# Kernel tuning notes

Hardware: AMD Instinct MI355X
Metric: run time of the kernel (lower is better)

The kernel has to match this reference:

```python
import jax, jax.numpy as jnp
import numpy as np

N_NODES = 100000
N_EDGES = 6400000


def setup_inputs() -> dict:
    key = jax.random.key(0)
    k1, k2, k3, k4, k5, k6 = jax.random.split(key, 6)
    x = jax.random.normal(k1, (N_NODES, 10), dtype=jnp.float32)
    edge_index = jax.random.randint(k2, (2, N_EDGES), 0, N_NODES, dtype=jnp.int64)
    # GCNConv(10,16) and GCNConv(16,2) parameters (glorot-ish scale)
    W1 = jax.random.normal(k3, (10, 16), dtype=jnp.float32) * (1.0 / np.sqrt(10))
    b1 = jnp.zeros((16,), dtype=jnp.float32)
    W2 = jax.random.normal(k4, (16, 2), dtype=jnp.float32) * (1.0 / np.sqrt(16))
    b2 = jnp.zeros((2,), dtype=jnp.float32)
    return {"x": x, "edge_index": edge_index, "W1": W1, "b1": b1, "W2": W2, "b2": b2}


def _gcn_conv(h, src, dst, norm, W, b, n_nodes):
    # PyG GCNConv: linear first, then normalized scatter-add aggregation
    h = h @ W                                   # [N, out]
    msg = h[src] * norm[:, None]                # gather + per-edge scale
    out = jax.ops.segment_sum(msg, dst, num_segments=n_nodes)
    return out + b


def reference(x, edge_index, W1, b1, W2, b2):
    n_nodes = x.shape[0]
    loop = jnp.arange(n_nodes, dtype=edge_index.dtype)
    src = jnp.concatenate([edge_index[0], loop])  # self-loops added (PyG default)
    dst = jnp.concatenate([edge_index[1], loop])
    # symmetric normalization deg^{-1/2} A_hat deg^{-1/2} (deg from target index)
    deg = jax.ops.segment_sum(jnp.ones_like(dst, dtype=x.dtype), dst, num_segments=n_nodes)
    dinv = jnp.where(deg > 0, jax.lax.rsqrt(deg), 0.0)
    norm = dinv[src] * dinv[dst]                 # [E+N]
    h = _gcn_conv(x, src, dst, norm, W1, b1, n_nodes)
    h = jax.nn.relu(h)
    out = _gcn_conv(h, src, dst, norm, W2, b2, n_nodes)
    return out
```

## Files before the change

kernel.cpp:

```cpp
#include <hip/hip_runtime.h>
#include <hip/hip_fp16.h>


#define BKT_BITS  8
#define BKT_SZ    256
#define NBK       512
#define TPB_A     1024
#define TPB_B     1024
#define CHUNK     25600
#define NIT       (CHUNK / TPB_A)
#define DST_SHIFT 24
#define SRC_MASK  0xFFFFFFu
#define XS_BYTES  32
#define SENTINEL  0xFFFFFFFFu

static __device__ __forceinline__ int nt_src(const void* ei, int is64, int n_edges, unsigned e) {
    return is64 ? (int)__builtin_nontemporal_load(&((const long long*)ei)[e])
                : __builtin_nontemporal_load(&((const int*)ei)[e]);
}
static __device__ __forceinline__ int nt_dst(const void* ei, int is64, int n_edges, unsigned e) {
    return is64 ? (int)__builtin_nontemporal_load(&((const long long*)ei)[(unsigned)n_edges + e])
                : __builtin_nontemporal_load(&((const int*)ei)[(unsigned)n_edges + e]);
}

static __device__ __forceinline__ float2 h2f(unsigned w) {
    __half2 h = *(__half2*)&w;
    return __half22float2(h);
}

static __global__ void detect_init_kernel(const unsigned int* __restrict__ w, int* flag,
                                          unsigned* __restrict__ gbase, unsigned cap) {
    __shared__ int nz;
    if (threadIdx.x == 0) nz = 0;
    __syncthreads();
    int local = 0;
    for (int k = threadIdx.x; k < 4096; k += blockDim.x)
        if (w[2 * k + 1] != 0u) local = 1;
    if (local) atomicOr(&nz, 1);
    __syncthreads();
    if (threadIdx.x == 0) *flag = (nz == 0) ? 1 : 0;
    for (int b = threadIdx.x; b < NBK; b += blockDim.x)
        gbase[b] = (unsigned)b * cap;
}

static __global__ void scatterB_kernel(const void* __restrict__ ei, const int* __restrict__ flag,
                                       unsigned* __restrict__ gbase,
                                       unsigned* __restrict__ bucketed,
                                       int n_edges, unsigned cap) {
    __shared__ unsigned short dlo[CHUNK];
    __shared__ unsigned dbit[CHUNK / 32];
    __shared__ unsigned h[NBK];
    __shared__ unsigned runbase[NBK];
    __shared__ unsigned cur[NBK];
    const int t = threadIdx.x;
    const unsigned e0 = (unsigned)blockIdx.x * CHUNK;
    const int is64 = *flag;
    for (int i = t; i < NBK; i += TPB_A) h[i] = 0u;
    __syncthreads();
    for (int it = 0; it < NIT; ++it) {
        unsigned idx = (unsigned)it * TPB_A + (unsigned)t;
        unsigned e = e0 + idx;
        bool valid = e < (unsigned)n_edges;
        unsigned d = valid ? (unsigned)nt_dst(ei, is64, n_edges, e) : 0u;
        dlo[idx] = (unsigned short)d;
        unsigned long long m = __ballot((d >> 16) & 1u);
        if ((t & 31) == 0)
            dbit[idx >> 5] = (unsigned)(((t & 63) >= 32) ? (m >> 32) : m);
        if (valid) atomicAdd(&h[d >> BKT_BITS], 1u);
    }
    __syncthreads();
    for (int b = t; b < NBK; b += TPB_A) {
        unsigned hb = h[b];
        unsigned rb = 0u;
        if (hb) rb = atomicAdd(&gbase[b], (hb + 15u) & ~15u);
        runbase[b] = rb;
        cur[b] = rb;
    }
    __syncthreads();
    for (int it = 0; it < NIT; ++it) {
        unsigned idx = (unsigned)it * TPB_A + (unsigned)t;
        unsigned e = e0 + idx;
        if (e < (unsigned)n_edges) {
            unsigned s = (unsigned)nt_src(ei, is64, n_edges, e);
            unsigned d = (unsigned)dlo[idx] | (((dbit[idx >> 5] >> (idx & 31u)) & 1u) << 16);
            unsigned b = d >> BKT_BITS;
            unsigned pos = atomicAdd(&cur[b], 1u);
            if (pos < (b + 1u) * cap)
                bucketed[pos] = s | ((d & (BKT_SZ - 1u)) << DST_SHIFT);
        }
    }
    __syncthreads();
    for (int b = t; b < NBK; b += TPB_A) {
        if (!h[b]) continue;
        unsigned rb = runbase[b];
        unsigned lim = (b + 1u) * cap;
        unsigned cu = cur[b]; if (cu > lim) cu = lim;
        unsigned end = rb + ((cu - rb + 15u) & ~15u);
        if (end > lim) end = lim;
        for (unsigned q = cu; q < end; ++q) bucketed[q] = SENTINEL;
    }
}

static __global__ void passB_kernel(const unsigned* __restrict__ bucketed,
                                    const unsigned* __restrict__ gbase, unsigned cap,
                                    const float* __restrict__ x,
                                    unsigned* __restrict__ csr_src,
                                    unsigned* __restrict__ row_start,
                                    unsigned* __restrict__ cnt,
                                    float* __restrict__ dinv,
                                    char* __restrict__ xs, int n_nodes) {
    const int b = blockIdx.x;
    const int n0 = b << BKT_BITS;
    const int t = threadIdx.x;
    const unsigned base = (unsigned)b * cap;
    unsigned gb = gbase[b];
    unsigned lim = base + cap;
    if (gb > lim) gb = lim;
    const unsigned count = gb - base;

    __shared__ unsigned h4[4][BKT_SZ];
    __shared__ unsigned s0[BKT_SZ], s1[BKT_SZ];
    __shared__ unsigned cur[BKT_SZ];
    for (int i = t; i < 4 * BKT_SZ; i += TPB_B) ((unsigned*)h4)[i] = 0u;
    __syncthreads();
    const int copy = (t >> 8) & 3;
    const uint4* B4 = (const uint4*)(bucketed + base);
    const unsigned nquad = count >> 2;
    for (unsigned q = t; q < nquad; q += TPB_B) {
        uint4 w4 = B4[q];
        if (w4.x != SENTINEL) atomicAdd(&h4[copy][w4.x >> DST_SHIFT], 1u);
        if (w4.y != SENTINEL) atomicAdd(&h4[copy][w4.y >> DST_SHIFT], 1u);
        if (w4.z != SENTINEL) atomicAdd(&h4[copy][w4.z >> DST_SHIFT], 1u);
        if (w4.w != SENTINEL) atomicAdd(&h4[copy][w4.w >> DST_SHIFT], 1u);
    }
    __syncthreads();
    unsigned hv = 0;
    unsigned* a = s0; unsigned* c = s1;
    if (t < BKT_SZ) {
        hv = h4[0][t] + h4[1][t] + h4[2][t] + h4[3][t];
        a[t] = hv;
    }
    __syncthreads();
    for (int off = 1; off < BKT_SZ; off <<= 1) {
        if (t < BKT_SZ) c[t] = a[t] + (t >= off ? a[t - off] : 0u);
        __syncthreads();
        unsigned* tmp = a; a = c; c = tmp;
    }
    if (t < BKT_SZ) {
        unsigned excl = a[t] - hv;
        cur[t] = excl;
        int n = n0 + t;
        if (n < n_nodes) {
            row_start[n] = base + excl;
            cnt[n] = hv;
            float di = rsqrtf((float)(hv + 1u));
            dinv[n] = di;
            unsigned w[5];
#pragma unroll
            for (int j = 0; j < 5; j++) {
                unsigned lo = __half_as_ushort(__float2half_rn(x[(size_t)n * 10 + 2 * j] * di));
                unsigned hi = __half_as_ushort(__float2half_rn(x[(size_t)n * 10 + 2 * j + 1] * di));
                w[j] = lo | (hi << 16);
            }
            char* row = xs + (size_t)n * XS_BYTES;
            *(uint4*)row = make_uint4(w[0], w[1], w[2], w[3]);
            *(uint2*)(row + 16) = make_uint2(w[4], 0u);
        }
    }
    __syncthreads();
    for (unsigned q = t; q < nquad; q += TPB_B) {
        uint4 w4 = B4[q];
        if (w4.x != SENTINEL) {
            unsigned pos = base + atomicAdd(&cur[w4.x >> DST_SHIFT], 1u);
            csr_src[pos] = w4.x & SRC_MASK;
        }
        if (w4.y != SENTINEL) {
            unsigned pos = base + atomicAdd(&cur[w4.y >> DST_SHIFT], 1u);
            csr_src[pos] = w4.y & SRC_MASK;
        }
        if (w4.z != SENTINEL) {
            unsigned pos = base + atomicAdd(&cur[w4.z >> DST_SHIFT], 1u);
            csr_src[pos] = w4.z & SRC_MASK;
        }
        if (w4.w != SENTINEL) {
            unsigned pos = base + atomicAdd(&cur[w4.w >> DST_SHIFT], 1u);
            csr_src[pos] = w4.w & SRC_MASK;
        }
    }
}

static __global__ void node1_kernel(const float* __restrict__ x, const float* __restrict__ dinv,
                                    char* __restrict__ xs, int n_nodes) {
    int i = blockIdx.x * blockDim.x + threadIdx.x;
    if (i >= n_nodes) return;
    float di = dinv[i];
    unsigned w[5];
#pragma unroll
    for (int j = 0; j < 5; j++) {
        unsigned lo = __half_as_ushort(__float2half_rn(x[(size_t)i * 10 + 2 * j] * di));
        unsigned hi = __half_as_ushort(__float2half_rn(x[(size_t)i * 10 + 2 * j + 1] * di));
        w[j] = lo | (hi << 16);
    }
    char* row = xs + (size_t)i * XS_BYTES;
    *(uint4*)row = make_uint4(w[0], w[1], w[2], w[3]);
    *(uint2*)(row + 16) = make_uint2(w[4], 0u);
}

static __global__ void gather1_kernel(const unsigned int* __restrict__ row_start,
                                      const unsigned int* __restrict__ cnt,
                                      const unsigned int* __restrict__ csr_src,
                                      const char* __restrict__ xs,
                                      const float* __restrict__ dinv,
                                      const float* __restrict__ W1, const float* __restrict__ b1,
                                      const float* __restrict__ W2,
                                      float* __restrict__ gs, int n_nodes) {
    __shared__ float sW1[160];
    __shared__ float sb1[16];
    __shared__ float sW2[32];
    for (int k = threadIdx.x; k < 160; k += blockDim.x) sW1[k] = W1[k];
    if (threadIdx.x < 16) sb1[threadIdx.x] = b1[threadIdx.x];
    if (threadIdx.x < 32) sW2[threadIdx.x] = W2[threadIdx.x];
    __syncthreads();
    int node = blockIdx.x * (blockDim.x >> 4) + (threadIdx.x >> 4);
    int lg = threadIdx.x & 15;
    if (node >= n_nodes) return;
    unsigned start = row_start[node];
    unsigned degn = cnt[node];
    float acc[10];
#pragma unroll
    for (int j = 0; j < 10; j++) acc[j] = 0.f;
    for (unsigned k = lg; k < degn; k += 16) {
        unsigned s = csr_src[start + k];
        const char* row = xs + (size_t)s * XS_BYTES;
        uint4 a = *(const uint4*)row;
        unsigned b = *(const unsigned*)(row + 16);
        float2 f;
        f = h2f(a.x); acc[0] += f.x; acc[1] += f.y;
        f = h2f(a.y); acc[2] += f.x; acc[3] += f.y;
        f = h2f(a.z); acc[4] += f.x; acc[5] += f.y;
        f = h2f(a.w); acc[6] += f.x; acc[7] += f.y;
        f = h2f(b);   acc[8] += f.x; acc[9] += f.y;
    }
    if (lg == 0) {
        const char* row = xs + (size_t)node * XS_BYTES;
        uint4 a = *(const uint4*)row;
        unsigned b = *(const unsigned*)(row + 16);
        float2 f;
        f = h2f(a.x); acc[0] += f.x; acc[1] += f.y;
        f = h2f(a.y); acc[2] += f.x; acc[3] += f.y;
        f = h2f(a.z); acc[4] += f.x; acc[5] += f.y;
        f = h2f(a.w); acc[6] += f.x; acc[7] += f.y;
        f = h2f(b);   acc[8] += f.x; acc[9] += f.y;
    }
#pragma unroll
    for (int off = 8; off > 0; off >>= 1) {
#pragma unroll
        for (int j = 0; j < 10; j++) acc[j] += __shfl_xor(acc[j], off);
    }
    float di = dinv[node];
    float h = sb1[lg];
#pragma unroll
    for (int k = 0; k < 10; k++) h = fmaf(acc[k] * di, sW1[k * 16 + lg], h);
    h = fmaxf(h, 0.f);
    float g0 = h * sW2[lg * 2 + 0];
    float g1 = h * sW2[lg * 2 + 1];
#pragma unroll
    for (int off = 8; off > 0; off >>= 1) {
        g0 += __shfl_xor(g0, off);
        g1 += __shfl_xor(g1, off);
    }
    if (lg == 0) {
        float2 o;
        o.x = g0 * di;
        o.y = g1 * di;
        ((float2*)gs)[node] = o;
    }
}

static __global__ void gather2_kernel(const unsigned int* __restrict__ row_start,
                                      const unsigned int* __restrict__ cnt,
                                      const unsigned int* __restrict__ csr_src,
                                      const float* __restrict__ gs,
                                      const float* __restrict__ dinv,
                                      const float* __restrict__ b2,
                                      float* __restrict__ out, int n_nodes) {
    int node = blockIdx.x * (blockDim.x >> 4) + (threadIdx.x >> 4);
    int lg = threadIdx.x & 15;
    if (node >= n_nodes) return;
    unsigned start = row_start[node];
    unsigned degn = cnt[node];
    float a0 = 0.f, a1 = 0.f;
    const float2* G = (const float2*)gs;
    for (unsigned k = lg; k < degn; k += 16) {
        float2 v = G[csr_src[start + k]];
        a0 += v.x; a1 += v.y;
    }
    if (lg == 0) {
        float2 s = G[node];
        a0 += s.x; a1 += s.y;
    }
#pragma unroll
    for (int off = 8; off > 0; off >>= 1) {
        a0 += __shfl_xor(a0, off);
        a1 += __shfl_xor(a1, off);
    }
    if (lg == 0) {
        float di = dinv[node];
        float2 o;
        o.x = fmaf(a0, di, b2[0]);
        o.y = fmaf(a1, di, b2[1]);
        ((float2*)out)[node] = o;
    }
}

static __global__ void deg_kernel(const void* __restrict__ ei, const int* __restrict__ flag,
                                  unsigned int* __restrict__ cnt, int n_edges) {
    const int is64 = *flag;
    unsigned stride = gridDim.x * blockDim.x;
    for (unsigned e = blockIdx.x * blockDim.x + threadIdx.x; e < (unsigned)n_edges; e += stride) {
        int d = nt_dst(ei, is64, n_edges, e);
        atomicAdd(&cnt[d], 1u);
    }
}
static __global__ void alloc_kernel(const unsigned int* __restrict__ cnt,
                                    unsigned int* __restrict__ row_start,
                                    unsigned int* __restrict__ cursor,
                                    unsigned int* __restrict__ gcur,
                                    float* __restrict__ dinv, int n_nodes) {
    __shared__ unsigned wsum[4];
    int i = blockIdx.x * blockDim.x + threadIdx.x;
    int lane = threadIdx.x & 63;
    int wid = threadIdx.x >> 6;
    unsigned d = (i < n_nodes) ? cnt[i] : 0u;
    unsigned scan = d;
#pragma unroll
    for (int off = 1; off < 64; off <<= 1) {
        unsigned t = __shfl_up(scan, off);
        if (lane >= off) scan += t;
    }
    if (lane == 63) wsum[wid] = scan;
    __syncthreads();
    if (threadIdx.x == 0) {
        unsigned s0 = wsum[0], s1 = wsum[1], s2 = wsum[2], s3 = wsum[3];
        unsigned base = atomicAdd(gcur, s0 + s1 + s2 + s3);
        wsum[0] = base;
        wsum[1] = base + s0;
        wsum[2] = base + s0 + s1;
        wsum[3] = base + s0 + s1 + s2;
    }
    __syncthreads();
    if (i < n_nodes) {
        unsigned pos = wsum[wid] + scan - d;
        row_start[i] = pos;
        cursor[i] = pos;
        dinv[i] = rsqrtf((float)(d + 1u));
    }
}
static __global__ void csrfill_kernel(const void* __restrict__ ei, const int* __restrict__ flag,
                                      unsigned int* __restrict__ cursor,
                                      unsigned int* __restrict__ csr_src, int n_edges) {
    const int is64 = *flag;
    unsigned stride = gridDim.x * blockDim.x;
    for (unsigned e = blockIdx.x * blockDim.x + threadIdx.x; e < (unsigned)n_edges; e += stride) {
        int s = nt_src(ei, is64, n_edges, e);
        int d = nt_dst(ei, is64, n_edges, e);
        unsigned pos = atomicAdd(&cursor[d], 1u);
        csr_src[pos] = (unsigned)s;
    }
}

static inline char* align_up(char* p, size_t a) {
    return (char*)(((uintptr_t)p + a - 1) & ~(uintptr_t)(a - 1));
}

extern "C" void kernel_launch(void* const* d_in, const int* in_sizes, int n_in,
                              void* d_out, int out_size, void* d_ws, size_t ws_size,
                              hipStream_t stream) {
    const float* x  = (const float*)d_in[0];
    const void*  ei = d_in[1];
    const float* W1 = (const float*)d_in[2];
    const float* b1 = (const float*)d_in[3];
    const float* W2 = (const float*)d_in[4];
    const float* b2 = (const float*)d_in[5];
    float* out = (float*)d_out;

    const int n_nodes = in_sizes[0] / 10;
    const int n_edges = in_sizes[1] / 2;
    (void)n_in; (void)out_size;

    const int nbuckets = (n_nodes + BKT_SZ - 1) >> BKT_BITS;
    const bool pack_ok = (n_nodes <= (1 << 17)) && (nbuckets <= NBK);
    const unsigned cap = (unsigned)(((((size_t)n_edges / (size_t)(nbuckets > 0 ? nbuckets : 1)) * 5 / 4)
                                     + 2048 + 15) & ~(size_t)15);
    const size_t region_words = (size_t)nbuckets * cap + 64;

    char* p = (char*)d_ws;
    int* flag = (int*)p;
    unsigned* gcur = (unsigned*)(p + 64);
    p += 256;
    unsigned* row_start = (unsigned*)p; p = align_up(p + (size_t)n_nodes * 4, 256);
    unsigned* cnt = (unsigned*)p;       p = align_up(p + (size_t)n_nodes * 4, 256);
    float* dinv = (float*)p;            p = align_up(p + (size_t)n_nodes * 4, 256);
    float* gs = (float*)p;              p = align_up(p + (size_t)n_nodes * 8, 256);
    char* xs = p;                       p = align_up(p + (size_t)n_nodes * XS_BYTES, 256);

    const size_t head_bytes = (size_t)(p - (char*)d_ws);
    const size_t need_new = head_bytes + 2 * (region_words * 4 + 256) + NBK * 4 + 256;
    const size_t need_old = head_bytes + (size_t)n_edges * 4 + 256 +
                            (size_t)n_nodes * 4 + 256;

    const int NODES_PER_BLK = 256 / 16;
    const int gblocks = (n_nodes + NODES_PER_BLK - 1) / NODES_PER_BLK;

    if (pack_ok && ws_size >= need_new) {
        unsigned* csr_src = (unsigned*)p;  p = align_up(p + region_words * 4, 256);
        unsigned* gbase = (unsigned*)p;    p = align_up(p + (size_t)NBK * 4, 256);
        unsigned* bucketed = (unsigned*)p; p = align_up(p + region_words * 4, 256);

        const int nblocksB = (int)(((unsigned)n_edges + CHUNK - 1) / CHUNK);

        detect_init_kernel<<<1, 256, 0, stream>>>((const unsigned int*)ei, flag, gbase, cap);
        scatterB_kernel<<<nblocksB, TPB_A, 0, stream>>>(ei, flag, gbase, bucketed, n_edges, cap);
        passB_kernel<<<nbuckets, TPB_B, 0, stream>>>(bucketed, gbase, cap, x, csr_src,
                                                     row_start, cnt, dinv, xs, n_nodes);
        gather1_kernel<<<gblocks, 256, 0, stream>>>(row_start, cnt, csr_src, xs, dinv,
                                                    W1, b1, W2, gs, n_nodes);
        gather2_kernel<<<gblocks, 256, 0, stream>>>(row_start, cnt, csr_src, gs, dinv,
                                                    b2, out, n_nodes);
    } else if (ws_size >= need_old) {
        unsigned* csr_src = (unsigned*)p; p = align_up(p + (size_t)n_edges * 4, 256);
        unsigned* cursor = (unsigned*)p;

        hipMemsetAsync(d_ws, 0, 256, stream);
        hipMemsetAsync(cnt, 0, (size_t)n_nodes * 4, stream);
        detect_init_kernel<<<1, 256, 0, stream>>>((const unsigned int*)ei, flag, gcur, 0u);
        deg_kernel<<<2048, 256, 0, stream>>>(ei, flag, cnt, n_edges);
        alloc_kernel<<<(n_nodes + 255) / 256, 256, 0, stream>>>(cnt, row_start, cursor, gcur, dinv, n_nodes);
        csrfill_kernel<<<4096, 256, 0, stream>>>(ei, flag, cursor, csr_src, n_edges);
        node1_kernel<<<(n_nodes + 255) / 256, 256, 0, stream>>>(x, dinv, xs, n_nodes);
        gather1_kernel<<<gblocks, 256, 0, stream>>>(row_start, cnt, csr_src, xs, dinv,
                                                    W1, b1, W2, gs, n_nodes);
        gather2_kernel<<<gblocks, 256, 0, stream>>>(row_start, cnt, csr_src, gs, dinv,
                                                    b2, out, n_nodes);
    }
}
```

Measured before the change: 199.9 us.

## Cache bucket words in LDS for second pass and unroll gather loops

In passB, the first part of each bucket's words is staged into a 56KB shared-memory cache during the histogram pass, so the scatter pass reads it from LDS instead of reloading it from global memory. The histogram replicas drop from four to two to make room. The gather kernels are unrolled to issue two or four independent index and row loads per iteration, which raises memory-level parallelism. The larger shared-memory footprint may lower occupancy in passB, and the fallback path now passes cnt instead of gcur to detect_init, which looks inconsistent.

```diff
diff --git a/kernel.cpp b/kernel.cpp
--- a/kernel.cpp
+++ b/kernel.cpp
@@ -13,6 +13,7 @@
 #define SRC_MASK  0xFFFFFFu
 #define XS_BYTES  32
 #define SENTINEL  0xFFFFFFFFu
+#define CACHE_W   14336
 
 static __device__ __forceinline__ int nt_src(const void* ei, int is64, int n_edges, unsigned e) {
     return is64 ? (int)__builtin_nontemporal_load(&((const long long*)ei)[e])
@@ -118,26 +119,30 @@
     if (gb > lim) gb = lim;
     const unsigned count = gb - base;
 
-    __shared__ unsigned h4[4][BKT_SZ];
+    __shared__ unsigned cacheW[CACHE_W];
+    __shared__ unsigned h2[2][BKT_SZ];
     __shared__ unsigned s0[BKT_SZ], s1[BKT_SZ];
     __shared__ unsigned cur[BKT_SZ];
-    for (int i = t; i < 4 * BKT_SZ; i += TPB_B) ((unsigned*)h4)[i] = 0u;
-    __syncthreads();
-    const int copy = (t >> 8) & 3;
+    for (int i = t; i < 2 * BKT_SZ; i += TPB_B) ((unsigned*)h2)[i] = 0u;
+    __syncthreads();
+    const int copy = (t >> 9) & 1;
     const uint4* B4 = (const uint4*)(bucketed + base);
+    uint4* C4 = (uint4*)cacheW;
     const unsigned nquad = count >> 2;
+    const unsigned cquad = CACHE_W >> 2;
     for (unsigned q = t; q < nquad; q += TPB_B) {
         uint4 w4 = B4[q];
-        if (w4.x != SENTINEL) atomicAdd(&h4[copy][w4.x >> DST_SHIFT], 1u);
-        if (w4.y != SENTINEL) atomicAdd(&h4[copy][w4.y >> DST_SHIFT], 1u);
-        if (w4.z != SENTINEL) atomicAdd(&h4[copy][w4.z >> DST_SHIFT], 1u);
-        if (w4.w != SENTINEL) atomicAdd(&h4[copy][w4.w >> DST_SHIFT], 1u);
+        if (q < cquad) C4[q] = w4;
+        if (w4.x != SENTINEL) atomicAdd(&h2[copy][w4.x >> DST_SHIFT], 1u);
+        if (w4.y != SENTINEL) atomicAdd(&h2[copy][w4.y >> DST_SHIFT], 1u);
+        if (w4.z != SENTINEL) atomicAdd(&h2[copy][w4.z >> DST_SHIFT], 1u);
+        if (w4.w != SENTINEL) atomicAdd(&h2[copy][w4.w >> DST_SHIFT], 1u);
     }
     __syncthreads();
     unsigned hv = 0;
     unsigned* a = s0; unsigned* c = s1;
     if (t < BKT_SZ) {
-        hv = h4[0][t] + h4[1][t] + h4[2][t] + h4[3][t];
+        hv = h2[0][t] + h2[1][t];
         a[t] = hv;
     }
     __syncthreads();
@@ -169,7 +174,7 @@
     }
     __syncthreads();
     for (unsigned q = t; q < nquad; q += TPB_B) {
-        uint4 w4 = B4[q];
+        uint4 w4 = (q < cquad) ? C4[q] : B4[q];
         if (w4.x != SENTINEL) {
             unsigned pos = base + atomicAdd(&cur[w4.x >> DST_SHIFT], 1u);
             csr_src[pos] = w4.x & SRC_MASK;
@@ -229,17 +234,30 @@
     float acc[10];
 #pragma unroll
     for (int j = 0; j < 10; j++) acc[j] = 0.f;
-    for (unsigned k = lg; k < degn; k += 16) {
-        unsigned s = csr_src[start + k];
-        const char* row = xs + (size_t)s * XS_BYTES;
-        uint4 a = *(const uint4*)row;
-        unsigned b = *(const unsigned*)(row + 16);
+    for (unsigned k = lg; k < degn; k += 32) {
+        unsigned s0 = csr_src[start + k];
+        unsigned k1 = k + 16;
+        bool v1 = k1 < degn;
+        unsigned s1 = v1 ? csr_src[start + k1] : s0;
+        const char* r0 = xs + (size_t)s0 * XS_BYTES;
+        const char* r1 = xs + (size_t)s1 * XS_BYTES;
+        uint4 a0 = *(const uint4*)r0;
+        unsigned b0 = *(const unsigned*)(r0 + 16);
+        uint4 a1 = *(const uint4*)r1;
+        unsigned b1w = *(const unsigned*)(r1 + 16);
         float2 f;
-        f = h2f(a.x); acc[0] += f.x; acc[1] += f.y;
-        f = h2f(a.y); acc[2] += f.x; acc[3] += f.y;
-        f = h2f(a.z); acc[4] += f.x; acc[5] += f.y;
-        f = h2f(a.w); acc[6] += f.x; acc[7] += f.y;
-        f = h2f(b);   acc[8] += f.x; acc[9] += f.y;
+        f = h2f(a0.x); acc[0] += f.x; acc[1] += f.y;
+        f = h2f(a0.y); acc[2] += f.x; acc[3] += f.y;
+        f = h2f(a0.z); acc[4] += f.x; acc[5] += f.y;
+        f = h2f(a0.w); acc[6] += f.x; acc[7] += f.y;
+        f = h2f(b0);   acc[8] += f.x; acc[9] += f.y;
+        if (v1) {
+            f = h2f(a1.x); acc[0] += f.x; acc[1] += f.y;
+            f = h2f(a1.y); acc[2] += f.x; acc[3] += f.y;
+            f = h2f(a1.z); acc[4] += f.x; acc[5] += f.y;
+            f = h2f(a1.w); acc[6] += f.x; acc[7] += f.y;
+            f = h2f(b1w);  acc[8] += f.x; acc[9] += f.y;
+        }
     }
     if (lg == 0) {
         const char* row = xs + (size_t)node * XS_BYTES;
@@ -291,9 +309,21 @@
     unsigned degn = cnt[node];
     float a0 = 0.f, a1 = 0.f;
     const float2* G = (const float2*)gs;
-    for (unsigned k = lg; k < degn; k += 16) {
-        float2 v = G[csr_src[start + k]];
-        a0 += v.x; a1 += v.y;
+    for (unsigned k = lg; k < degn; k += 64) {
+        unsigned k1 = k + 16, k2 = k + 32, k3 = k + 48;
+        bool v1 = k1 < degn, v2 = k2 < degn, v3 = k3 < degn;
+        unsigned s0 = csr_src[start + k];
+        unsigned s1 = v1 ? csr_src[start + k1] : s0;
+        unsigned s2 = v2 ? csr_src[start + k2] : s0;
+        unsigned s3 = v3 ? csr_src[start + k3] : s0;
+        float2 w0 = G[s0];
+        float2 w1 = G[s1];
+        float2 w2 = G[s2];
+        float2 w3 = G[s3];
+        a0 += w0.x; a1 += w0.y;
+        if (v1) { a0 += w1.x; a1 += w1.y; }
+        if (v2) { a0 += w2.x; a1 += w2.y; }
+        if (v3) { a0 += w3.x; a1 += w3.y; }
     }
     if (lg == 0) {
         float2 s = G[node];
@@ -433,7 +463,7 @@
 
         hipMemsetAsync(d_ws, 0, 256, stream);
         hipMemsetAsync(cnt, 0, (size_t)n_nodes * 4, stream);
-        detect_init_kernel<<<1, 256, 0, stream>>>((const unsigned int*)ei, flag, gcur, 0u);
+        detect_init_kernel<<<1, 256, 0, stream>>>((const unsigned int*)ei, flag, cnt, 0u);
         deg_kernel<<<2048, 256, 0, stream>>>(ei, flag, cnt, n_edges);
         alloc_kernel<<<(n_nodes + 255) / 256, 256, 0, stream>>>(cnt, row_start, cursor, gcur, dinv, n_nodes);
         csrfill_kernel<<<4096, 256, 0, stream>>>(ei, flag, cursor, csr_src, n_edges);
```

New measurement: 196.8 us. About the same (-1.5%).
